# Performance work log

Measured on AMD Instinct MI355X. Metric: run time of the kernel, lower is better.

Reference implementation:

```python
import jax, jax.numpy as jnp
import numpy as np

HEADS = 16

def setup_inputs() -> dict:
    key = jax.random.key(0)
    ks = jax.random.split(key, 5)
    B, N, C = 2, 2048, 1024
    s = 0.02
    return {
        "x": jax.random.normal(ks[0], (B, N, C), jnp.float32),
        "y": jax.random.normal(ks[1], (B, N, C), jnp.float32),
        "w_qkv": jax.random.normal(ks[2], (C, 3 * C), jnp.float32) * s,  # acts as Linear weight^T
        "w_proj": jax.random.normal(ks[3], (C, C), jnp.float32) * s,
        "b_proj": jnp.zeros((C,), jnp.float32),
    }

def _qkv_heads(t, w_qkv, B, N, H, D):
    qkv = (t @ w_qkv).reshape(B, N, 3, H, D)
    qkv = jnp.transpose(qkv, (2, 0, 3, 1, 4))  # [3, B, H, N, D]
    return qkv[0], qkv[1], qkv[2]

def reference(x, y, w_qkv, w_proj, b_proj):
    B, N, C = x.shape
    H = HEADS
    D = C // H
    scale = D ** (-0.5)
    q, k, v = _qkv_heads(x, w_qkv, B, N, H, D)
    q1, k1, v1 = _qkv_heads(y, w_qkv, B, N, H, D)
    attn = jax.nn.softmax(jnp.einsum('bhnd,bhmd->bhnm', q, k) * scale, axis=-1)
    attn1 = jax.nn.softmax(jnp.einsum('bhnd,bhmd->bhnm', q1, k1) * scale, axis=-1)
    # cross-swapped values: x-branch attends over v1 (from y), y-branch over v (from x)
    ox = jnp.einsum('bhnm,bhmd->bhnd', attn, v1)
    oy = jnp.einsum('bhnm,bhmd->bhnd', attn1, v)
    ox = jnp.transpose(ox, (0, 2, 1, 3)).reshape(B, N, C)
    oy = jnp.transpose(oy, (0, 2, 1, 3)).reshape(B, N, C)
    x_out = ox @ w_proj + b_proj + x
    y_out = oy @ w_proj + b_proj + y
    return x_out, y_out
```

## Files before the change

kernel.cpp:

```cpp
#include <hip/hip_runtime.h>

using u16    = unsigned short;
using short8 = __attribute__((ext_vector_type(8))) short;
using f32x4  = __attribute__((ext_vector_type(4))) float;
using f32x16 = __attribute__((ext_vector_type(16))) float;

#define MFMA16(a, b, c) __builtin_amdgcn_mfma_f32_16x16x32_bf16(a, b, c, 0, 0, 0)
#define MFMA32(a, b, c) __builtin_amdgcn_mfma_f32_32x32x16_bf16(a, b, c, 0, 0, 0)

#define QSCALE 0.18033688011112042f

__device__ inline u16 f2bf(float f) {
  union { float f; unsigned u; } v; v.f = f;
  unsigned r = v.u + 0x7fffu + ((v.u >> 16) & 1u);
  return (u16)(r >> 16);
}

__device__ __forceinline__ void load_lds16(const u16* g, u16* l) {
  __builtin_amdgcn_global_load_lds((const __attribute__((address_space(1))) void*)g,
                                   (__attribute__((address_space(3))) void*)l, 16, 0, 0);
}

__device__ __forceinline__ unsigned cvt_pk_bf16(float lo, float hi) {
  unsigned r;
  asm("v_cvt_pk_bf16_f32 %0, %1, %2" : "=v"(r) : "v"(lo), "v"(hi));
  return r;
}

__device__ __forceinline__ void plswap(unsigned& a, unsigned& b) {
  auto r = __builtin_amdgcn_permlane32_swap(a, b, false, false);
  a = r[0];
  b = r[1];
}

__global__ __launch_bounds__(256) void cvt_k(const float* __restrict__ src,
                                             u16* __restrict__ dst) {
  const int i = (blockIdx.x * 256 + threadIdx.x) * 8;
  const float4 a = *(const float4*)&src[i];
  const float4 b = *(const float4*)&src[i + 4];
  short8 o;
  o[0] = (short)f2bf(a.x); o[1] = (short)f2bf(a.y);
  o[2] = (short)f2bf(a.z); o[3] = (short)f2bf(a.w);
  o[4] = (short)f2bf(b.x); o[5] = (short)f2bf(b.y);
  o[6] = (short)f2bf(b.z); o[7] = (short)f2bf(b.w);
  *(short8*)&dst[i] = o;
}

__global__ __launch_bounds__(256) void cvtT_k(const float* __restrict__ src,
                                              u16* __restrict__ dst, int R, int C) {
  __shared__ float t[64][65];
  const int c0 = blockIdx.x * 64, r0 = blockIdx.y * 64;
  const int lc = threadIdx.x & 63, g = threadIdx.x >> 6;
#pragma unroll
  for (int i = 0; i < 16; ++i) {
    const int r = g + i * 4;
    t[r][lc] = src[(size_t)(r0 + r) * C + c0 + lc];
  }
  __syncthreads();
#pragma unroll
  for (int i = 0; i < 16; ++i) {
    const int c = g + i * 4;
    dst[(size_t)(c0 + c) * R + r0 + lc] = f2bf(t[lc][c]);
  }
}

template <int MODE>
__global__ __launch_bounds__(256, 2) void gemm_k(
    const u16* __restrict__ A0, const u16* __restrict__ A1,
    const u16* __restrict__ Bt,
    u16* __restrict__ q_out, u16* __restrict__ k_out, u16* __restrict__ v_out,
    float* __restrict__ c0, float* __restrict__ c1,
    const float* __restrict__ bias,
    const float* __restrict__ res0, const float* __restrict__ res1) {
  __shared__ alignas(16) u16 lA[128 * 64];
  __shared__ alignas(16) u16 lB[128 * 64];
  const int z = blockIdx.z;
  const u16* A = z ? A1 : A0;
  float* c_out = z ? c1 : c0;
  const float* res = z ? res1 : res0;
  const int head_base = z * 32;

  const int tid = threadIdx.x;
  const int lane = tid & 63, wave = tid >> 6;
  const int quad = lane >> 4, l16 = lane & 15;
  const int lsw = (l16 & 7) * 8;
  const int wm = (wave >> 1) * 64, wn = (wave & 1) * 64;
  const int bn0 = blockIdx.x * 128, bm0 = blockIdx.y * 128;
  const int srow = lane >> 3;
  const int sg = (lane & 7) ^ srow;

  f32x4 acc[4][4] = {};

  for (int k0 = 0; k0 < 1024; k0 += 64) {
    __syncthreads();
#pragma unroll
    for (int it = 0; it < 4; ++it) {
      const int rb = wave * 32 + it * 8;
      const int r = rb + srow;
      load_lds16(&A[(size_t)(bm0 + r) * 1024 + k0 + sg * 8], &lA[rb * 64]);
      load_lds16(&Bt[(size_t)(bn0 + r) * 1024 + k0 + sg * 8], &lB[rb * 64]);
    }
    asm volatile("s_waitcnt vmcnt(0)" ::: "memory");
    __syncthreads();
#pragma unroll
    for (int kt = 0; kt < 2; ++kt) {
      short8 af[4], bfr[4];
#pragma unroll
      for (int i = 0; i < 4; ++i) {
        const int go = ((kt * 4 + quad) * 8) ^ lsw;
        af[i]  = *(const short8*)&lA[(wm + i * 16 + l16) * 64 + go];
        bfr[i] = *(const short8*)&lB[(wn + i * 16 + l16) * 64 + go];
      }
#pragma unroll
      for (int i = 0; i < 4; ++i)
#pragma unroll
        for (int j = 0; j < 4; ++j)
          acc[i][j] = MFMA16(af[i], bfr[j], acc[i][j]);
    }
  }

#pragma unroll
  for (int i = 0; i < 4; ++i) {
    const int row = bm0 + wm + i * 16 + quad * 4;
#pragma unroll
    for (int j = 0; j < 4; ++j) {
      const int col = bn0 + wn + j * 16 + l16;
#pragma unroll
      for (int r = 0; r < 4; ++r) {
        const float v = acc[i][j][r];
        const int m = row + r;
        if (MODE == 0) {
          const int which = col >> 10;
          const int h = (col >> 6) & 15, d = col & 63;
          const int b = m >> 11, n = m & 2047;
          const size_t hh = (size_t)(head_base + b * 16 + h);
          if (which == 0)      q_out[(hh * 2048 + n) * 64 + d] = f2bf(v * QSCALE);
          else if (which == 1) k_out[(hh * 2048 + n) * 64 + d] = f2bf(v);
          else                 v_out[(hh * 64 + d) * 2048 + n] = f2bf(v);
        } else {
          const size_t idx = (size_t)m * 1024 + col;
          c_out[idx] = v + bias[col] + res[idx];
        }
      }
    }
  }
}

__global__ __launch_bounds__(256, 4) void attn_k(const u16* __restrict__ Q,
                                                 const u16* __restrict__ K,
                                                 const u16* __restrict__ V,
                                                 u16* __restrict__ O) {
  __shared__ alignas(16) u16 kT[2][64 * 64];
  __shared__ alignas(16) u16 vT[2][64 * 64];

  const int tid = threadIdx.x;
  const int lane = tid & 63, wave = tid >> 6;
  const int qn = lane & 31, h = lane >> 5;

  const int d0 = blockIdx.x;
  const int swz = ((d0 & 7) << 7) | (d0 >> 3);
  const int qx = swz & 15;
  const int hh = (swz >> 4) & 15;
  const int z  = swz >> 8;
  const int s = z >> 1, b = z & 1;

  const int head_qk = z * 16 + hh;
  const int head_v  = (z ^ 2) * 16 + hh;
  const u16* Qh = Q + (size_t)head_qk * 2048 * 64;
  const u16* Kh = K + (size_t)head_qk * 2048 * 64;
  const u16* Vh = V + (size_t)head_v * 64 * 2048;
  const int qr0 = qx * 128 + wave * 32;

  short8 qf[4];
#pragma unroll
  for (int f = 0; f < 4; ++f)
    qf[f] = *(const short8*)&Qh[(size_t)(qr0 + qn) * 64 + f * 16 + h * 8];

  f32x16 oacc[2] = {};
  float l_i = 0.f;

  const int srow = lane >> 3;

  union PU { unsigned u[4]; short8 s; };

  auto stage = [&](int buf, int j0) {
#pragma unroll
    for (int it = 0; it < 2; ++it) {
      const int rb = wave * 16 + it * 8;
      const int r = rb + srow;
      const int sgx = (lane & 7) ^ srow ^ (rb >> 3);
      load_lds16(&Kh[(size_t)(j0 + r) * 64 + sgx * 8], &kT[buf][rb * 64]);
      load_lds16(&Vh[(size_t)r * 2048 + j0 + sgx * 8], &vT[buf][rb * 64]);
    }
  };

  stage(0, 0);
  asm volatile("s_waitcnt vmcnt(0)" ::: "memory");
  __syncthreads();

  int cur = 0;
  for (int j0 = 0; j0 < 2048; j0 += 64) {
    if (j0 + 64 < 2048) stage(cur ^ 1, j0 + 64);
    const u16* kb = kT[cur];
    const u16* vb = vT[cur];

    f32x16 sacc[2] = {};
#pragma unroll
    for (int t = 0; t < 2; ++t) {
      const int row = t * 32 + qn;
      const int key = (row & 7) ^ (row >> 3);
#pragma unroll
      for (int kd = 0; kd < 4; ++kd) {
        const int go = ((kd * 2 + h) ^ key) * 8;
        const short8 kf = *(const short8*)&kb[row * 64 + go];
        sacc[t] = MFMA32(kf, qf[kd], sacc[t]);
      }
    }

    float rs = 0.f;
    unsigned pw[2][8];
#pragma unroll
    for (int t = 0; t < 2; ++t)
#pragma unroll
      for (int j = 0; j < 8; ++j) {
        const float pa0 = __builtin_amdgcn_exp2f(sacc[t][2 * j]);
        const float pa1 = __builtin_amdgcn_exp2f(sacc[t][2 * j + 1]);
        rs += pa0 + pa1;
        pw[t][j] = cvt_pk_bf16(pa0, pa1);
      }

    PU pa[4];
#pragma unroll
    for (int t = 0; t < 2; ++t)
#pragma unroll
      for (int e = 0; e < 2; ++e) {
        unsigned a0 = pw[t][4 * e + 0], a2 = pw[t][4 * e + 2];
        unsigned a1 = pw[t][4 * e + 1], a3 = pw[t][4 * e + 3];
        plswap(a0, a2);
        plswap(a1, a3);
        pa[2 * t + e].u[0] = a0; pa[2 * t + e].u[1] = a1;
        pa[2 * t + e].u[2] = a2; pa[2 * t + e].u[3] = a3;
      }

    rs += __shfl_xor(rs, 32, 64);
    l_i += rs;

#pragma unroll
    for (int dt = 0; dt < 2; ++dt) {
      const int row = dt * 32 + qn;
      const int key = (row & 7) ^ (row >> 3);
#pragma unroll
      for (int st = 0; st < 4; ++st) {
        const int go = ((st * 2 + h) ^ key) * 8;
        const short8 vf = *(const short8*)&vb[row * 64 + go];
        oacc[dt] = MFMA32(pa[st].s, vf, oacc[dt]);
      }
    }

    asm volatile("s_waitcnt vmcnt(0)" ::: "memory");
    __syncthreads();
    cur ^= 1;
  }

  u16* Ob = O + (size_t)s * 4096 * 1024;
#pragma unroll
  for (int r = 0; r < 16; ++r) {
    const int qrow = (r & 3) + 8 * (r >> 2) + 4 * h;
    const float lr = __shfl(l_i, qrow, 64);
    const float inv = 1.f / lr;
    const size_t base = (size_t)(b * 2048 + qr0 + qrow) * 1024 + hh * 64;
#pragma unroll
    for (int dt = 0; dt < 2; ++dt)
      Ob[base + dt * 32 + qn] = f2bf(oacc[dt][r] * inv);
  }
}

extern "C" void kernel_launch(void* const* d_in, const int* in_sizes, int n_in,
                              void* d_out, int out_size, void* d_ws, size_t ws_size,
                              hipStream_t stream) {
  const float* x      = (const float*)d_in[0];
  const float* y      = (const float*)d_in[1];
  const float* w_qkv  = (const float*)d_in[2];
  const float* w_proj = (const float*)d_in[3];
  const float* b_proj = (const float*)d_in[4];
  float* out = (float*)d_out;

  u16* xb     = (u16*)d_ws;
  u16* yb     = xb + 4194304;
  u16* Ob     = xb;
  u16* wqkvT  = yb + 4194304;
  u16* wprojT = wqkvT + 3145728;
  u16* Qs     = wprojT + 1048576;
  u16* Ks     = Qs + 8388608;
  u16* Vs     = Ks + 8388608;

  cvt_k<<<2048, 256, 0, stream>>>(x, xb);
  cvt_k<<<2048, 256, 0, stream>>>(y, yb);
  cvtT_k<<<dim3(48, 16), 256, 0, stream>>>(w_qkv, wqkvT, 1024, 3072);
  cvtT_k<<<dim3(16, 16), 256, 0, stream>>>(w_proj, wprojT, 1024, 1024);

  gemm_k<0><<<dim3(24, 32, 2), 256, 0, stream>>>(xb, yb, wqkvT, Qs, Ks, Vs,
                                                 nullptr, nullptr, nullptr,
                                                 nullptr, nullptr);

  attn_k<<<1024, 256, 0, stream>>>(Qs, Ks, Vs, Ob);

  gemm_k<1><<<dim3(8, 32, 2), 256, 0, stream>>>(Ob, Ob + 4194304, wprojT,
                                                nullptr, nullptr, nullptr,
                                                out, out + 4194304, b_proj, x, y);
}
```

Baseline: 296.2 us.

## Add 256x256-tile 8-wave pipelined GEMM for the QKV projection

Replaces the QKV projection GEMM with a new kernel using 256x256 output tiles, 512 threads (8 waves) and double-buffered LDS filled through direct global-to-LDS loads. Loads are split into half-tiles interleaved with MFMA phases under fine-grained barriers and vmcnt waits. The larger tile raises arithmetic intensity and the interleaving hides load latency. In exchange it uses more LDS and registers per block, which lowers occupancy, and the grid is small (384 blocks), which may leave CUs unevenly loaded.

Result: slower. 304.8 us (+2.9%).

```diff
diff --git a/kernel.cpp b/kernel.cpp
--- a/kernel.cpp
+++ b/kernel.cpp
@@ -9,6 +9,10 @@
 #define MFMA32(a, b, c) __builtin_amdgcn_mfma_f32_32x32x16_bf16(a, b, c, 0, 0, 0)
 
 #define QSCALE 0.18033688011112042f
+
+#define BAR do { asm volatile("" ::: "memory"); __builtin_amdgcn_s_barrier(); \
+                 asm volatile("" ::: "memory"); } while (0)
+#define VMW(N) asm volatile("s_waitcnt vmcnt(" #N ")" ::: "memory")
 
 __device__ inline u16 f2bf(float f) {
   union { float f; unsigned u; } v; v.f = f;
@@ -146,6 +150,136 @@
   }
 }
 
+__device__ __forceinline__ void rdA256(short8 (&af)[2][4], const u16* half,
+                                       int rh, int l16, int quad) {
+#pragma unroll
+  for (int kk = 0; kk < 2; ++kk)
+#pragma unroll
+    for (int i = 0; i < 4; ++i) {
+      const int rowh = rh * 64 + i * 16 + l16;
+      const int go = ((kk * 4 + quad) ^ (l16 & 7)) * 8;
+      af[kk][i] = *(const short8*)&half[rowh * 64 + go];
+    }
+}
+__device__ __forceinline__ void rdB256(short8 (&bf)[2][2], const u16* half,
+                                       int ch, int wn1, int l16, int quad) {
+#pragma unroll
+  for (int kk = 0; kk < 2; ++kk)
+#pragma unroll
+    for (int j = 0; j < 2; ++j) {
+      const int colh = wn1 * 64 + ch * 32 + j * 16 + l16;
+      const int go = ((kk * 4 + quad) ^ (l16 & 7)) * 8;
+      bf[kk][j] = *(const short8*)&half[colh * 64 + go];
+    }
+}
+template <int RH, int CH>
+__device__ __forceinline__ void mm256(f32x4 (&acc)[8][4], const short8 (&af)[2][4],
+                                      const short8 (&bf)[2][2]) {
+#pragma unroll
+  for (int kk = 0; kk < 2; ++kk)
+#pragma unroll
+    for (int i = 0; i < 4; ++i)
+#pragma unroll
+      for (int j = 0; j < 2; ++j)
+        acc[RH * 4 + i][CH * 2 + j] =
+            MFMA16(af[kk][i], bf[kk][j], acc[RH * 4 + i][CH * 2 + j]);
+}
+
+__global__ __launch_bounds__(512, 2) void gemm256_k(
+    const u16* __restrict__ A0, const u16* __restrict__ A1,
+    const u16* __restrict__ Bt,
+    u16* __restrict__ q_out, u16* __restrict__ k_out, u16* __restrict__ v_out) {
+  __shared__ alignas(16) u16 lds[2][2][2][128 * 64];
+  const int z = blockIdx.z;
+  const u16* A = z ? A1 : A0;
+  const int head_base = z * 32;
+
+  const int tid = threadIdx.x;
+  const int lane = tid & 63, wave = tid >> 6;
+  const int wm = wave >> 2, wn = wave & 3;
+  const int wn1 = wn & 1;
+  const int quad = lane >> 4, l16 = lane & 15;
+  const int bn0 = blockIdx.x * 256, bm0 = blockIdx.y * 256;
+  const int srow = lane >> 3;
+  const int sg = (lane & 7) ^ srow;
+
+  const u16* dA[2] = { &lds[0][0][wm][0], &lds[1][0][wm][0] };
+  const u16* dB[2] = { &lds[0][1][wn >> 1][0], &lds[1][1][wn >> 1][0] };
+
+  f32x4 acc[8][4] = {};
+
+  auto stg = [&](int buf, int mat, int half, int kt) {
+    const u16* src = mat ? Bt : A;
+    const int gb = mat ? bn0 : bm0;
+#pragma unroll
+    for (int L = 0; L < 2; ++L) {
+      const int rb = wave * 16 + L * 8;
+      const int r = half * 128 + rb + srow;
+      load_lds16(&src[(size_t)(gb + r) * 1024 + kt * 64 + sg * 8],
+                 &lds[buf][mat][half][rb * 64]);
+    }
+  };
+
+  stg(0, 1, 0, 0); stg(0, 1, 1, 0); stg(0, 0, 0, 0); stg(0, 0, 1, 0);
+  stg(1, 1, 0, 1); stg(1, 1, 1, 1);
+  VMW(4); BAR;
+
+  short8 af[2][4], bf0[2][2], bf1[2][2];
+#pragma unroll 1
+  for (int i = 0; i < 8; ++i) {
+    const int b   = 2 * i + 1;
+    const int kt2 = (2 * i + 2) & 15;
+    const int kt3 = (2 * i + 3) & 15;
+    rdA256(af, dA[0], 0, l16, quad);
+    rdB256(bf0, dB[0], 0, wn1, l16, quad);
+    stg(1, 0, 0, b);
+    BAR; mm256<0, 0>(acc, af, bf0); BAR;
+    rdB256(bf1, dB[0], 1, wn1, l16, quad);
+    stg(1, 0, 1, b);
+    BAR; mm256<0, 1>(acc, af, bf1); BAR;
+    rdA256(af, dA[0], 1, l16, quad);
+    stg(0, 1, 0, kt2);
+    BAR; mm256<1, 0>(acc, af, bf0); BAR;
+    stg(0, 1, 1, kt2);
+    VMW(4);
+    BAR; mm256<1, 1>(acc, af, bf1); BAR;
+    rdA256(af, dA[1], 0, l16, quad);
+    rdB256(bf0, dB[1], 0, wn1, l16, quad);
+    stg(0, 0, 0, kt2);
+    BAR; mm256<0, 0>(acc, af, bf0); BAR;
+    rdB256(bf1, dB[1], 1, wn1, l16, quad);
+    stg(0, 0, 1, kt2);
+    BAR; mm256<0, 1>(acc, af, bf1); BAR;
+    rdA256(af, dA[1], 1, l16, quad);
+    stg(1, 1, 0, kt3);
+    BAR; mm256<1, 0>(acc, af, bf0); BAR;
+    stg(1, 1, 1, kt3);
+    VMW(4);
+    BAR; mm256<1, 1>(acc, af, bf1); BAR;
+  }
+
+#pragma unroll
+  for (int ri = 0; ri < 8; ++ri) {
+    const int row = bm0 + wm * 128 + ri * 16 + quad * 4;
+#pragma unroll
+    for (int cj = 0; cj < 4; ++cj) {
+      const int col = bn0 + wn * 64 + cj * 16 + l16;
+      const int which = col >> 10;
+      const int hcol = (col >> 6) & 15, d = col & 63;
+#pragma unroll
+      for (int r = 0; r < 4; ++r) {
+        const float v = acc[ri][cj][r];
+        const int m = row + r;
+        const int bb = m >> 11, n = m & 2047;
+        const size_t hh = (size_t)(head_base + bb * 16 + hcol);
+        if (which == 0)      q_out[(hh * 2048 + n) * 64 + d] = f2bf(v * QSCALE);
+        else if (which == 1) k_out[(hh * 2048 + n) * 64 + d] = f2bf(v);
+        else                 v_out[(hh * 64 + d) * 2048 + n] = f2bf(v);
+      }
+    }
+  }
+}
+
 __global__ __launch_bounds__(256, 4) void attn_k(const u16* __restrict__ Q,
                                                  const u16* __restrict__ K,
                                                  const u16* __restrict__ V,
@@ -299,9 +433,7 @@
   cvtT_k<<<dim3(48, 16), 256, 0, stream>>>(w_qkv, wqkvT, 1024, 3072);
   cvtT_k<<<dim3(16, 16), 256, 0, stream>>>(w_proj, wprojT, 1024, 1024);
 
-  gemm_k<0><<<dim3(24, 32, 2), 256, 0, stream>>>(xb, yb, wqkvT, Qs, Ks, Vs,
-                                                 nullptr, nullptr, nullptr,
-                                                 nullptr, nullptr);
+  gemm256_k<<<dim3(12, 16, 2), 512, 0, stream>>>(xb, yb, wqkvT, Qs, Ks, Vs);
 
   attn_k<<<1024, 256, 0, stream>>>(Qs, Ks, Vs, Ob);
 
```
